# Optimization experiments

Hardware: AMD Instinct MI355X
Metric: run time of the kernel (lower is better)

## Reference

```python
import jax, jax.numpy as jnp
import numpy as np

LOWER_CURV = -0.22703196
UPPER_CURV = 0.36853024
N_NODES = 50000
N_EDGES = 400000
KSIZE = 5            # kernel_size per dim
KTOT = KSIZE ** 3    # 125 weight matrices (dim=3)
DIMS = [1, 8, 16, 16, 8, 1]
# corner bit patterns for degree-1 B-spline in 3D: [8,3]
_BITS = np.array([[(s >> d) & 1 for d in range(3)] for s in range(8)], dtype=np.int32)


def transform(x, rng=10.0):
    t = (x - LOWER_CURV) / (UPPER_CURV - LOWER_CURV) * (2.0 * rng) - rng
    return jnp.clip(t, -rng, rng)


def spline_basis(pseudo):
    # pseudo: [E,3] in [0,1]. Degree-1 open B-spline, kernel_size=5 per dim.
    pos = jnp.clip(pseudo, 0.0, 1.0) * (KSIZE - 1)                  # [E,3]
    k0 = jnp.clip(jnp.floor(pos), 0, KSIZE - 2).astype(jnp.int32)   # [E,3]
    frac = pos - k0.astype(pos.dtype)                               # [E,3]
    bits = jnp.asarray(_BITS)                                       # [8,3]
    # basis[e,s] = prod_d (frac_d if bit else 1-frac_d)
    basis = jnp.prod(jnp.where(bits[None, :, :] == 1, frac[:, None, :], 1.0 - frac[:, None, :]), axis=-1)  # [E,8]
    idx = k0[:, None, :] + bits[None, :, :]                         # [E,8,3]
    wi = idx[..., 0] * (KSIZE * KSIZE) + idx[..., 1] * KSIZE + idx[..., 2]  # [E,8] in [0,125)
    return basis, wi


def spline_conv(x, src, dst, basis, wi, weight, root, bias):
    # x: [N,Cin]; weight: [125,Cin,Cout]; sum aggregation (norm=False)
    n, cin = x.shape
    xs = x[src]                                          # [E,Cin] gather
    contrib = basis[..., None] * xs[:, None, :]          # [E,8,Cin]
    seg = (dst[:, None] * KTOT + wi).reshape(-1)         # [8E] combined (node,kernel) id
    h = jax.ops.segment_sum(contrib.reshape(-1, cin), seg, num_segments=n * KTOT)
    out = jnp.einsum('vki,kio->vo', h.reshape(n, KTOT, cin), weight)
    return out + x @ root + bias


def setup_inputs() -> dict:
    key = jax.random.key(0)
    ks = jax.random.split(key, 20)
    inp = {}
    inp['x'] = jax.random.normal(ks[0], (N_NODES, 1), dtype=jnp.float32) * 0.2
    inp['edge_index'] = jax.random.randint(ks[1], (2, N_EDGES), 0, N_NODES, dtype=jnp.int32)
    inp['edge_attr'] = jax.random.uniform(ks[2], (N_EDGES, 3), dtype=jnp.float32)
    for l in range(5):
        cin, cout = DIMS[l], DIMS[l + 1]
        inp[f'w{l+1}'] = jax.random.normal(ks[3 + 3 * l], (KTOT, cin, cout), dtype=jnp.float32) / np.sqrt(8.0 * cin)
        inp[f'root{l+1}'] = jax.random.normal(ks[4 + 3 * l], (cin, cout), dtype=jnp.float32) / np.sqrt(float(cin))
        inp[f'b{l+1}'] = jnp.zeros((cout,), dtype=jnp.float32)
    return inp


def reference(x, edge_index, edge_attr, w1, root1, b1, w2, root2, b2, w3, root3, b3, w4, root4, b4, w5, root5, b5):
    src, dst = edge_index[0], edge_index[1]
    basis, wi = spline_basis(edge_attr)
    h = transform(x, 10.0)
    for (w, r, b) in ((w1, root1, b1), (w2, root2, b2), (w3, root3, b3), (w4, root4, b4), (w5, root5, b5)):
        h = jax.nn.elu(spline_conv(h, src, dst, basis, wi, w, r, b))
    return h.reshape(-1)
```

## Files before the change

kernel.cpp:

```cpp
#include <hip/hip_runtime.h>
#include <math.h>

#define KSIZE 5
#define KTOT 125
#define CHUNK 2048

static constexpr float LOWER_CURV = -0.22703196f;
static constexpr float UPPER_CURV = 0.36853024f;

typedef _Float16 h2 __attribute__((ext_vector_type(2)));
typedef _Float16 h8_t __attribute__((ext_vector_type(8)));
typedef float f32x4 __attribute__((ext_vector_type(4)));

__device__ __forceinline__ unsigned pack_u32(float a, float b) {
    return __builtin_bit_cast(unsigned, __builtin_amdgcn_cvt_pkrtz(a, b));
}

__host__ __device__ static inline int cdiv(int a, int b) { return (a + b - 1) / b; }

__device__ __forceinline__ void unpack_bb10(unsigned w1, float bb[8]) {
    const float s = 1.0f / 1023.0f;
    float f0 = (float)(w1 & 1023u) * s;
    float f1 = (float)((w1 >> 10) & 1023u) * s;
    float f2 = (float)((w1 >> 20) & 1023u) * s;
    float a0 = 1.f - f0, a1 = 1.f - f1, a2 = 1.f - f2;
    float p00 = a0 * a1, p10 = f0 * a1, p01 = a0 * f1, p11 = f0 * f1;
    bb[0] = p00 * a2; bb[1] = p10 * a2; bb[2] = p01 * a2; bb[3] = p11 * a2;
    bb[4] = p00 * f2; bb[5] = p10 * f2; bb[6] = p01 * f2; bb[7] = p11 * f2;
}

__device__ __forceinline__ void spline_wf(const float* __restrict__ a3,
                                          int& wib, float fr[3]) {
    int k[3];
#pragma unroll
    for (int d = 0; d < 3; ++d) {
        float p = fminf(fmaxf(a3[d], 0.f), 1.f) * 4.f;
        float f0 = fminf(floorf(p), 3.f);
        k[d] = (int)f0;
        fr[d] = p - f0;
    }
    wib = k[0] * 25 + k[1] * 5 + k[2];
}


__global__ void zero_counts(int* __restrict__ p, int n) {
    int i = blockIdx.x * blockDim.x + threadIdx.x;
    if (i < n) p[i] = 0;
}

__global__ __launch_bounds__(256) void hist_tr(
        const float* __restrict__ x, float* __restrict__ h,
        const int* __restrict__ dst, const float* __restrict__ attr,
        int* __restrict__ counts, int* __restrict__ bcnt, int N, int E) {
    __shared__ int lh[KTOT];
    const int tid = threadIdx.x;
    for (int i = tid; i < KTOT; i += 256) lh[i] = 0;
    __syncthreads();
    int i = blockIdx.x * 256 + tid;
    if (i < N) {
        float t = (x[i] - LOWER_CURV) / (UPPER_CURV - LOWER_CURV) * 20.0f - 10.0f;
        h[i] = fminf(fmaxf(t, -10.0f), 10.0f);
    }
    const int base = blockIdx.x * CHUNK;
#pragma unroll
    for (int k = 0; k < 8; ++k) {
        int e = base + tid + k * 256;
        if (e < E) {
            atomicAdd(&counts[dst[e]], 1);
            float a3[3] = {attr[e * 3], attr[e * 3 + 1], attr[e * 3 + 2]};
            int wib; float fr[3];
            spline_wf(a3, wib, fr);
            atomicAdd(&lh[wib], 1);
        }
    }
    __syncthreads();
    for (int j = tid; j < KTOT; j += 256) {
        int c = lh[j];
        if (c) atomicAdd(&bcnt[j], c);
    }
}

__global__ void scan_blocks(const int* __restrict__ counts, int* __restrict__ rowptr,
                            int* __restrict__ bsums, int n) {
    __shared__ int sh[256];
    int tid = threadIdx.x;
    int i = blockIdx.x * 256 + tid;
    int v = (i < n) ? counts[i] : 0;
    sh[tid] = v;
    __syncthreads();
    for (int off = 1; off < 256; off <<= 1) {
        int t = (tid >= off) ? sh[tid - off] : 0;
        __syncthreads();
        sh[tid] += t;
        __syncthreads();
    }
    if (i < n) rowptr[i] = sh[tid] - v;
    if (tid == 255) bsums[blockIdx.x] = sh[255];
}

__global__ void add_offsets2(int* __restrict__ rowptr, const int* __restrict__ bsums,
                             int* __restrict__ cursor, const int* __restrict__ bcnt,
                             int* __restrict__ bases, int* __restrict__ bcursor,
                             int nb, int n, int E) {
    __shared__ int sh[256];
    __shared__ int sb[128];
    int tid = threadIdx.x;
    int v = (tid < nb) ? bsums[tid] : 0;
    sh[tid] = v;
    __syncthreads();
    for (int off = 1; off < 256; off <<= 1) {
        int t = (tid >= off) ? sh[tid - off] : 0;
        __syncthreads();
        sh[tid] += t;
        __syncthreads();
    }
    int boff = (blockIdx.x == 0) ? 0 : sh[blockIdx.x - 1];
    int i = blockIdx.x * 256 + tid;
    if (i < n) {
        int r = rowptr[i] + boff;
        rowptr[i] = r;
        cursor[i] = r;
    }
    if (i == 0) rowptr[n] = E;
    if (blockIdx.x == 0) {
        int cap = 0;
        if (tid < 128) {
            cap = (tid < KTOT) ? ((bcnt[tid] + 15) & ~15) : 0;
            sb[tid] = cap;
        }
        __syncthreads();
        for (int off = 1; off < 128; off <<= 1) {
            int t = (tid >= off && tid < 128) ? sb[tid - off] : 0;
            __syncthreads();
            if (tid < 128) sb[tid] += t;
            __syncthreads();
        }
        if (tid < KTOT) {
            int excl = sb[tid] - cap;
            bases[tid] = excl;
            bcursor[tid] = excl;
            if (tid == KTOT - 1) bases[KTOT] = excl + cap;
        }
    }
}

__global__ __launch_bounds__(256) void scatter_prep(
        const int* __restrict__ src, const int* __restrict__ dst,
        const float* __restrict__ attr, int* __restrict__ cursor,
        int* __restrict__ bcursor, const int* __restrict__ bcnt,
        const int* __restrict__ bases,
        uint2* __restrict__ records, uint2* __restrict__ records_d,
        int* __restrict__ iperm, int E, int nchunk, int nprep,
        const float* __restrict__ W2, const float* __restrict__ W3,
        const float* __restrict__ W4, _Float16* __restrict__ wh2,
        _Float16* __restrict__ wh3, _Float16* __restrict__ wh4) {
    __shared__ int lh[KTOT], lbase[KTOT], lrank[KTOT];
    const int tid = threadIdx.x;

    if ((int)blockIdx.x >= nchunk + nprep) {
        int b = (int)blockIdx.x - nchunk - nprep;
        int s = bases[b] + bcnt[b];
        int e = bases[b + 1];
        for (int i = s + tid; i < e; i += 256) {
            records[i] = make_uint2((unsigned)b << 18, 0u);
            iperm[i] = E;
        }
        return;
    }
    if ((int)blockIdx.x >= nchunk) {
        int idx = ((int)blockIdx.x - nchunk) * 256 + tid;
        if (idx >= 80000) return;
        if (idx < 16000) {
            int wi = idx / 128, q = idx % 128;
            int i = q / 16, o = q % 16;
            wh2[wi * 128 + o * 8 + i] = (_Float16)W2[idx];
        } else if (idx < 48000) {
            int r = idx - 16000;
            int wi = r / 256, q = r % 256;
            int i = q / 16, o = q % 16;
            wh3[wi * 256 + (i >> 3) * 128 + o * 8 + (i & 7)] = (_Float16)W3[r];
        } else {
            int r = idx - 48000;
            int wi = r / 256, q = r % 256;
            int i = q / 16, o = q % 16;
            float val = (o < 8) ? W4[(wi * 16 + i) * 8 + o] : 0.0f;
            wh4[wi * 256 + (i >> 3) * 128 + o * 8 + (i & 7)] = (_Float16)val;
        }
        return;
    }

    for (int i = tid; i < KTOT; i += 256) { lh[i] = 0; lrank[i] = 0; }
    __syncthreads();
    const int base = blockIdx.x * CHUNK;

    int wibs[8]; unsigned w1s[8];
#pragma unroll
    for (int k = 0; k < 8; ++k) {
        int e = base + tid + k * 256;
        wibs[k] = -1;
        if (e < E) {
            float a3[3] = {attr[e * 3], attr[e * 3 + 1], attr[e * 3 + 2]};
            int wib; float fr[3];
            spline_wf(a3, wib, fr);
            wibs[k] = wib;
            unsigned q0 = (unsigned)__float2int_rn(fr[0] * 1023.f);
            unsigned q1 = (unsigned)__float2int_rn(fr[1] * 1023.f);
            unsigned q2 = (unsigned)__float2int_rn(fr[2] * 1023.f);
            w1s[k] = q0 | (q1 << 10) | (q2 << 20);
            atomicAdd(&lh[wib], 1);
        }
    }
    __syncthreads();
    for (int i = tid; i < KTOT; i += 256) {
        int c = lh[i];
        lbase[i] = c ? atomicAdd(&bcursor[i], c) : 0;
    }
    __syncthreads();
#pragma unroll
    for (int k = 0; k < 8; ++k) {
        int e = base + tid + k * 256;
        if (e < E) {
            int w = wibs[k];
            int pos = lbase[w] + atomicAdd(&lrank[w], 1);
            uint2 rec = make_uint2((unsigned)src[e] | ((unsigned)w << 18), w1s[k]);
            records[pos] = rec;
            int p = atomicAdd(&cursor[dst[e]], 1);
            iperm[pos] = p;
            records_d[p] = rec;
        }
    }
}

template<int Cin, int CR>
__global__ __launch_bounds__(512) void edge_gemm_mfma(
        const uint2* __restrict__ records, const unsigned* __restrict__ xh,
        const _Float16* __restrict__ Wg, const int* __restrict__ iperm,
        _Float16* __restrict__ y, const int* __restrict__ epad_ptr) {
    constexpr int Cout = 16;
    constexpr int CC = Cin * Cout;
    constexpr int WH = KTOT * CC;
    constexpr int NM = Cin / 4;
    __shared__ __align__(16) _Float16 Wl[WH];
    for (int t = threadIdx.x; t < WH / 8; t += 512)
        ((uint4*)Wl)[t] = ((const uint4*)Wg)[t];
    __syncthreads();

    const int Ep = *epad_ptr;
    const int ntiles = Ep >> 4;
    const int lane = threadIdx.x & 63;
    const int o = lane & 15;
    const int kb = lane >> 4;
    const int chunk = (Cin == 16) ? (kb & 1) : 0;
    const int wid = blockIdx.x * 8 + (threadIdx.x >> 6);
    const int nwaves = gridDim.x * 8;
    constexpr int TAP[8] = {0, 25, 5, 30, 1, 26, 6, 31};

    for (int tile = wid; tile < ntiles; tile += nwaves) {
        const int tb = tile << 4;
        uint2 rec = records[tb + o];
        const int wib = (int)(((unsigned)__builtin_amdgcn_readfirstlane((int)rec.x)) >> 18);
        float bb[8];
        unpack_bb10(rec.y, bb);
        const unsigned sn = rec.x & 0x3FFFFu;
        uint4 xq = *(const uint4*)(xh + (size_t)sn * (Cin / 2) + chunk * 4);
        h2 xv[4];
        xv[0] = __builtin_bit_cast(h2, xq.x);
        xv[1] = __builtin_bit_cast(h2, xq.y);
        xv[2] = __builtin_bit_cast(h2, xq.z);
        xv[3] = __builtin_bit_cast(h2, xq.w);

        f32x4 acc = {0.f, 0.f, 0.f, 0.f};
#pragma unroll
        for (int m = 0; m < NM; ++m) {
            const int t = (Cin == 16) ? (2 * m + (kb >> 1)) : (4 * m + kb);
            const int wi = wib + TAP[t];
            _Float16 sh = (_Float16)bb[t];
            h2 ss; ss[0] = sh; ss[1] = sh;
            union { h8_t v; h2 h[4]; uint4 q; } A, B;
            A.h[0] = xv[0] * ss; A.h[1] = xv[1] * ss;
            A.h[2] = xv[2] * ss; A.h[3] = xv[3] * ss;
            B.q = *(const uint4*)&Wl[wi * CC + chunk * (8 * Cout) + o * 8];
            acc = __builtin_amdgcn_mfma_f32_16x16x32_f16(A.v, B.v, acc, 0, 0, 0);
        }
        if (CR == 16 || o < CR) {
#pragma unroll
            for (int r = 0; r < 4; ++r) {
                int dp = iperm[tb + kb * 4 + r];
                y[(size_t)dp * CR + o] = (_Float16)acc[r];
            }
        }
    }
}

template<int Cin, int Cout>
__global__ void node_reduce(const int* __restrict__ rowptr,
                            const unsigned* __restrict__ yu,
                            const float* __restrict__ x,
                            const float* __restrict__ root,
                            const float* __restrict__ bias,
                            float* __restrict__ out, unsigned* __restrict__ xh,
                            int N) {
    constexpr int C2 = Cout / 2;
    int t = blockIdx.x * blockDim.x + threadIdx.x;
    int v = t / C2, o2 = t % C2;
    if (v >= N) return;
    int beg = rowptr[v], end = rowptr[v + 1];
    float a0 = 0.f, a1 = 0.f;
    for (int p = beg; p < end; ++p) {
        h2 hh = __builtin_bit_cast(h2, yu[(size_t)p * C2 + o2]);
        a0 += (float)hh[0];
        a1 += (float)hh[1];
    }
    const int o = 2 * o2;
    a0 += bias[o]; a1 += bias[o + 1];
#pragma unroll
    for (int i = 0; i < Cin; ++i) {
        float xv = x[(size_t)v * Cin + i];
        a0 = fmaf(xv, root[i * Cout + o], a0);
        a1 = fmaf(xv, root[i * Cout + o + 1], a1);
    }
    a0 = a0 > 0.f ? a0 : expm1f(a0);
    a1 = a1 > 0.f ? a1 : expm1f(a1);
    ((float2*)out)[(size_t)v * C2 + o2] = make_float2(a0, a1);
    xh[(size_t)v * C2 + o2] = pack_u32(a0, a1);
}


__global__ __launch_bounds__(512) void agg_l1(
        const int* __restrict__ rowptr, const uint2* __restrict__ records_d,
        const float* __restrict__ x, const float* __restrict__ W,
        const float* __restrict__ root, const float* __restrict__ bias,
        float* __restrict__ out, unsigned* __restrict__ xh2,
        int N, int totalWaves) {
    const int lane = threadIdx.x & 63;
    const int o = lane & 7;
    const int slot = lane >> 3;
    const int wid = blockIdx.x * 8 + (threadIdx.x >> 6);
    constexpr int TAP[8] = {0, 25, 5, 30, 1, 26, 6, 31};

    for (int v = wid; v < N; v += totalWaves) {
        const int beg = rowptr[v], end = rowptr[v + 1];
        float acc = 0.0f;
        for (int p0 = beg; p0 < end; p0 += 8) {
            const int p = p0 + slot;
            float xv = 0.f, bb[8];
            int wib = 0;
#pragma unroll
            for (int t = 0; t < 8; ++t) bb[t] = 0.f;
            if (p < end) {
                uint2 rec = records_d[p];
                unpack_bb10(rec.y, bb);
                wib = (int)(rec.x >> 18);
                xv = x[rec.x & 0x3FFFFu];
            }
#pragma unroll
            for (int t = 0; t < 8; ++t)
                acc = fmaf(bb[t] * xv, __ldg(&W[(wib + TAP[t]) * 8 + o]), acc);
        }
#pragma unroll
        for (int m = 8; m < 64; m <<= 1) acc += __shfl_xor(acc, m);
        if (slot == 0) {
            float z = acc + bias[o] + x[v] * root[o];
            z = z > 0.0f ? z : expm1f(z);
            out[(size_t)v * 8 + o] = z;
            float zp = __shfl_xor(z, 1);
            if ((o & 1) == 0) xh2[(size_t)v * 4 + (o >> 1)] = pack_u32(z, zp);
        }
    }
}

__global__ __launch_bounds__(512) void agg_l5(
        const int* __restrict__ rowptr, const uint2* __restrict__ records_d,
        const float* __restrict__ x, const float* __restrict__ W,
        const float* __restrict__ root, const float* __restrict__ bias,
        float* __restrict__ out, int N, int totalWaves) {
    const int lane = threadIdx.x & 63;
    const int i = lane & 7;
    const int slot = lane >> 3;
    const int wid = blockIdx.x * 8 + (threadIdx.x >> 6);
    constexpr int TAP[8] = {0, 25, 5, 30, 1, 26, 6, 31};

    for (int v = wid; v < N; v += totalWaves) {
        const int beg = rowptr[v], end = rowptr[v + 1];
        float acc = 0.0f;
        for (int p0 = beg; p0 < end; p0 += 8) {
            const int p = p0 + slot;
            float xi = 0.f, bb[8];
            int wib = 0;
#pragma unroll
            for (int t = 0; t < 8; ++t) bb[t] = 0.f;
            if (p < end) {
                uint2 rec = records_d[p];
                unpack_bb10(rec.y, bb);
                wib = (int)(rec.x >> 18);
                xi = x[(size_t)(rec.x & 0x3FFFFu) * 8 + i];
            }
#pragma unroll
            for (int t = 0; t < 8; ++t)
                acc = fmaf(bb[t] * xi, __ldg(&W[(wib + TAP[t]) * 8 + i]), acc);
        }
        if (slot == 0) acc = fmaf(x[(size_t)v * 8 + i], root[i], acc);
#pragma unroll
        for (int m = 1; m < 64; m <<= 1) acc += __shfl_xor(acc, m);
        if (lane == 0) {
            float z = acc + bias[0];
            out[v] = z > 0.0f ? z : expm1f(z);
        }
    }
}


static inline char* align256(char* p) {
    return (char*)(((uintptr_t)p + 255) & ~(uintptr_t)255);
}

extern "C" void kernel_launch(void* const* d_in, const int* in_sizes, int n_in,
                              void* d_out, int out_size, void* d_ws, size_t ws_size,
                              hipStream_t stream) {
    const float* x    = (const float*)d_in[0];
    const int*   ei   = (const int*)d_in[1];
    const float* attr = (const float*)d_in[2];
    const float* w[5]    = {(const float*)d_in[3],  (const float*)d_in[6],
                            (const float*)d_in[9],  (const float*)d_in[12],
                            (const float*)d_in[15]};
    const float* root[5] = {(const float*)d_in[4],  (const float*)d_in[7],
                            (const float*)d_in[10], (const float*)d_in[13],
                            (const float*)d_in[16]};
    const float* bias[5] = {(const float*)d_in[5],  (const float*)d_in[8],
                            (const float*)d_in[11], (const float*)d_in[14],
                            (const float*)d_in[17]};

    const int N = in_sizes[0];
    const int E = in_sizes[1] / 2;
    const int* src = ei;
    const int* dst = ei + E;
    const int EPCAP = E + 2048;

    char* ws = (char*)d_ws;
    float* bufA      = (float*)ws;    ws = align256(ws + (size_t)N * 16 * 4);
    float* bufB      = (float*)ws;    ws = align256(ws + (size_t)N * 16 * 4);
    int*   counts    = (int*)ws;      ws = align256(ws + (size_t)(N + 128) * 4);
    int*   bcnt      = counts + N;
    int*   cursor    = (int*)ws;      ws = align256(ws + (size_t)N * 4);
    int*   rowptr    = (int*)ws;      ws = align256(ws + (size_t)(N + 1) * 4);
    int*   bsums     = (int*)ws;      ws = align256(ws + 256 * 4);
    int*   bases     = (int*)ws;      ws = align256(ws + 128 * 4);
    int*   bcursor   = (int*)ws;      ws = align256(ws + 128 * 4);
    uint2* records   = (uint2*)ws;    ws = align256(ws + (size_t)EPCAP * 8);
    uint2* records_d = (uint2*)ws;    ws = align256(ws + (size_t)E * 8);
    int*   iperm     = (int*)ws;      ws = align256(ws + (size_t)EPCAP * 4);
    _Float16* y      = (_Float16*)ws; ws = align256(ws + (size_t)(E + 16) * 16 * 2);
    unsigned* xhA    = (unsigned*)ws; ws = align256(ws + (size_t)N * 8 * 4);
    unsigned* xhB    = (unsigned*)ws; ws = align256(ws + (size_t)N * 8 * 4);
    _Float16* wh2    = (_Float16*)ws; ws = align256(ws + (size_t)KTOT * 8 * 16 * 2);
    _Float16* wh3    = (_Float16*)ws; ws = align256(ws + (size_t)KTOT * 16 * 16 * 2);
    _Float16* wh4    = (_Float16*)ws; ws = align256(ws + (size_t)KTOT * 16 * 16 * 2);

    const int B = 256;
    const int nb = cdiv(N, 256);
    const int nchunk = cdiv(E, CHUNK);
    const int nprep = cdiv(80000, 256);
    const int* epad = bases + KTOT;
    const unsigned* yu = (const unsigned*)y;

    zero_counts<<<cdiv(N + 128, B), B, 0, stream>>>(counts, N + 128);
    hist_tr<<<nchunk, 256, 0, stream>>>(x, bufA, dst, attr, counts, bcnt, N, E);
    scan_blocks<<<nb, 256, 0, stream>>>(counts, rowptr, bsums, N);
    add_offsets2<<<nb, 256, 0, stream>>>(rowptr, bsums, cursor, bcnt, bases,
                                         bcursor, nb, N, E);
    scatter_prep<<<nchunk + nprep + KTOT, 256, 0, stream>>>(
        src, dst, attr, cursor, bcursor, bcnt, bases,
        records, records_d, iperm, E, nchunk, nprep,
        w[1], w[2], w[3], wh2, wh3, wh4);

    const int GB = 512, TW = GB * 8;

    agg_l1<<<GB, 512, 0, stream>>>(rowptr, records_d, bufA, w[0],
                                   root[0], bias[0], bufB, xhA, N, TW);
    edge_gemm_mfma<8, 16><<<GB, 512, 0, stream>>>(records, xhA, wh2, iperm, y, epad);
    node_reduce<8, 16><<<cdiv(N * 8, B), B, 0, stream>>>(rowptr, yu, bufB,
                                                         root[1], bias[1], bufA, xhB, N);
    edge_gemm_mfma<16, 16><<<GB, 512, 0, stream>>>(records, xhB, wh3, iperm, y, epad);
    node_reduce<16, 16><<<cdiv(N * 8, B), B, 0, stream>>>(rowptr, yu, bufA,
                                                          root[2], bias[2], bufB, xhA, N);
    edge_gemm_mfma<16, 8><<<GB, 512, 0, stream>>>(records, xhA, wh4, iperm, y, epad);
    node_reduce<16, 8><<<cdiv(N * 4, B), B, 0, stream>>>(rowptr, yu, bufB,
                                                         root[3], bias[3], bufA, xhB, N);
    agg_l5<<<GB, 512, 0, stream>>>(rowptr, records_d, bufA, w[4],
                                   root[4], bias[4], (float*)d_out, N, TW);
}
```

Baseline: 175.5 us.

## Replace dst-sorted agg kernels for layers 1 and 5 with edge-then-reduce passes

Drops the dst-ordered records_d copy and its scattered write in scatter_prep. Layers 1 and 5 now use the same scheme as the middle layers: an edge-parallel kernel over the kernel-bucketed records writes per-edge messages through iperm, then a node reduce over rowptr sums them. This removes the per-node wave loops, which were badly load-balanced and read W through scattered global loads, and keeps the weights in LDS instead. The cost is an extra kernel launch per layer plus a round trip of intermediate messages through global memory, with fp16 rounding of the layer-1 messages and fp16 inputs and weights in layer 5.

```diff
diff --git a/kernel.cpp b/kernel.cpp
--- a/kernel.cpp
+++ b/kernel.cpp
@@ -14,6 +14,13 @@
 
 __device__ __forceinline__ unsigned pack_u32(float a, float b) {
     return __builtin_bit_cast(unsigned, __builtin_amdgcn_cvt_pkrtz(a, b));
+}
+__device__ __forceinline__ float fdot2f(h2 a, h2 b, float c) {
+#if __has_builtin(__builtin_amdgcn_fdot2)
+    return __builtin_amdgcn_fdot2(a, b, c, false);
+#else
+    return c + (float)a[0] * (float)b[0] + (float)a[1] * (float)b[1];
+#endif
 }
 
 __host__ __device__ static inline int cdiv(int a, int b) { return (a + b - 1) / b; }
@@ -149,8 +156,8 @@
         const float* __restrict__ attr, int* __restrict__ cursor,
         int* __restrict__ bcursor, const int* __restrict__ bcnt,
         const int* __restrict__ bases,
-        uint2* __restrict__ records, uint2* __restrict__ records_d,
-        int* __restrict__ iperm, int E, int nchunk, int nprep,
+        uint2* __restrict__ records, int* __restrict__ iperm,
+        int E, int nchunk, int nprep,
         const float* __restrict__ W2, const float* __restrict__ W3,
         const float* __restrict__ W4, _Float16* __restrict__ wh2,
         _Float16* __restrict__ wh3, _Float16* __restrict__ wh4) {
@@ -222,13 +229,99 @@
         if (e < E) {
             int w = wibs[k];
             int pos = lbase[w] + atomicAdd(&lrank[w], 1);
-            uint2 rec = make_uint2((unsigned)src[e] | ((unsigned)w << 18), w1s[k]);
-            records[pos] = rec;
-            int p = atomicAdd(&cursor[dst[e]], 1);
-            iperm[pos] = p;
-            records_d[p] = rec;
-        }
-    }
+            records[pos] = make_uint2((unsigned)src[e] | ((unsigned)w << 18), w1s[k]);
+            iperm[pos] = atomicAdd(&cursor[dst[e]], 1);
+        }
+    }
+}
+
+__global__ __launch_bounds__(512) void l1_edge(
+        const uint2* __restrict__ records, const float* __restrict__ h,
+        const float* __restrict__ W1,
+        const int* __restrict__ iperm, _Float16* __restrict__ y,
+        const int* __restrict__ epad_ptr) {
+    __shared__ float Wl[KTOT * 8];
+    for (int i = threadIdx.x; i < KTOT * 8; i += 512) Wl[i] = W1[i];
+    __syncthreads();
+    const int Ep = *epad_ptr;
+    const int stride = gridDim.x * 512;
+    constexpr int TAP[8] = {0, 25, 5, 30, 1, 26, 6, 31};
+    for (int idx = blockIdx.x * 512 + threadIdx.x; idx < Ep; idx += stride) {
+        uint2 rec = records[idx];
+        float bb[8];
+        unpack_bb10(rec.y, bb);
+        const int wib = (int)(rec.x >> 18);
+        float xv = h[rec.x & 0x3FFFFu];
+        float s[8];
+#pragma unroll
+        for (int o = 0; o < 8; ++o) s[o] = 0.f;
+#pragma unroll
+        for (int t = 0; t < 8; ++t) {
+            const float* wp = &Wl[(wib + TAP[t]) * 8];
+#pragma unroll
+            for (int o = 0; o < 8; ++o) s[o] = fmaf(bb[t], wp[o], s[o]);
+        }
+        uint4 pk;
+        pk.x = pack_u32(xv * s[0], xv * s[1]);
+        pk.y = pack_u32(xv * s[2], xv * s[3]);
+        pk.z = pack_u32(xv * s[4], xv * s[5]);
+        pk.w = pack_u32(xv * s[6], xv * s[7]);
+        int dp = iperm[idx];
+        *(uint4*)&y[(size_t)dp * 8] = pk;
+    }
+}
+
+__global__ __launch_bounds__(512) void l5_edge(
+        const uint2* __restrict__ records, const unsigned* __restrict__ xh,
+        const float* __restrict__ W5,
+        const int* __restrict__ iperm, float* __restrict__ y5,
+        const int* __restrict__ epad_ptr) {
+    __shared__ h2 Wl[KTOT * 4];
+    for (int i = threadIdx.x; i < KTOT * 4; i += 512)
+        Wl[i] = __builtin_bit_cast(h2, pack_u32(W5[2 * i], W5[2 * i + 1]));
+    __syncthreads();
+    const int Ep = *epad_ptr;
+    const int stride = gridDim.x * 512;
+    constexpr int TAP[8] = {0, 25, 5, 30, 1, 26, 6, 31};
+    for (int idx = blockIdx.x * 512 + threadIdx.x; idx < Ep; idx += stride) {
+        uint2 rec = records[idx];
+        float bb[8];
+        unpack_bb10(rec.y, bb);
+        const int wib = (int)(rec.x >> 18);
+        uint4 xq = *(const uint4*)(xh + (size_t)(rec.x & 0x3FFFFu) * 4);
+        h2 hx[4];
+        hx[0] = __builtin_bit_cast(h2, xq.x);
+        hx[1] = __builtin_bit_cast(h2, xq.y);
+        hx[2] = __builtin_bit_cast(h2, xq.z);
+        hx[3] = __builtin_bit_cast(h2, xq.w);
+        float acc = 0.f;
+#pragma unroll
+        for (int t = 0; t < 8; ++t) {
+            const h2* wp = &Wl[(wib + TAP[t]) * 4];
+            float dot = 0.f;
+            dot = fdot2f(hx[0], wp[0], dot);
+            dot = fdot2f(hx[1], wp[1], dot);
+            dot = fdot2f(hx[2], wp[2], dot);
+            dot = fdot2f(hx[3], wp[3], dot);
+            acc = fmaf(bb[t], dot, acc);
+        }
+        y5[iperm[idx]] = acc;
+    }
+}
+
+__global__ void node_fin5(const int* __restrict__ rowptr, const float* __restrict__ y5,
+                          const float* __restrict__ x,
+                          const float* __restrict__ root, const float* __restrict__ bias,
+                          float* __restrict__ out, int N) {
+    int v = blockIdx.x * blockDim.x + threadIdx.x;
+    if (v >= N) return;
+    int beg = rowptr[v], end = rowptr[v + 1];
+    float acc = bias[0];
+    for (int p = beg; p < end; ++p) acc += y5[p];
+#pragma unroll
+    for (int i = 0; i < 8; ++i)
+        acc = fmaf(x[(size_t)v * 8 + i], root[i], acc);
+    out[v] = acc > 0.f ? acc : expm1f(acc);
 }
 
 template<int Cin, int CR>
@@ -326,90 +419,6 @@
 }
 
 
-__global__ __launch_bounds__(512) void agg_l1(
-        const int* __restrict__ rowptr, const uint2* __restrict__ records_d,
-        const float* __restrict__ x, const float* __restrict__ W,
-        const float* __restrict__ root, const float* __restrict__ bias,
-        float* __restrict__ out, unsigned* __restrict__ xh2,
-        int N, int totalWaves) {
-    const int lane = threadIdx.x & 63;
-    const int o = lane & 7;
-    const int slot = lane >> 3;
-    const int wid = blockIdx.x * 8 + (threadIdx.x >> 6);
-    constexpr int TAP[8] = {0, 25, 5, 30, 1, 26, 6, 31};
-
-    for (int v = wid; v < N; v += totalWaves) {
-        const int beg = rowptr[v], end = rowptr[v + 1];
-        float acc = 0.0f;
-        for (int p0 = beg; p0 < end; p0 += 8) {
-            const int p = p0 + slot;
-            float xv = 0.f, bb[8];
-            int wib = 0;
-#pragma unroll
-            for (int t = 0; t < 8; ++t) bb[t] = 0.f;
-            if (p < end) {
-                uint2 rec = records_d[p];
-                unpack_bb10(rec.y, bb);
-                wib = (int)(rec.x >> 18);
-                xv = x[rec.x & 0x3FFFFu];
-            }
-#pragma unroll
-            for (int t = 0; t < 8; ++t)
-                acc = fmaf(bb[t] * xv, __ldg(&W[(wib + TAP[t]) * 8 + o]), acc);
-        }
-#pragma unroll
-        for (int m = 8; m < 64; m <<= 1) acc += __shfl_xor(acc, m);
-        if (slot == 0) {
-            float z = acc + bias[o] + x[v] * root[o];
-            z = z > 0.0f ? z : expm1f(z);
-            out[(size_t)v * 8 + o] = z;
-            float zp = __shfl_xor(z, 1);
-            if ((o & 1) == 0) xh2[(size_t)v * 4 + (o >> 1)] = pack_u32(z, zp);
-        }
-    }
-}
-
-__global__ __launch_bounds__(512) void agg_l5(
-        const int* __restrict__ rowptr, const uint2* __restrict__ records_d,
-        const float* __restrict__ x, const float* __restrict__ W,
-        const float* __restrict__ root, const float* __restrict__ bias,
-        float* __restrict__ out, int N, int totalWaves) {
-    const int lane = threadIdx.x & 63;
-    const int i = lane & 7;
-    const int slot = lane >> 3;
-    const int wid = blockIdx.x * 8 + (threadIdx.x >> 6);
-    constexpr int TAP[8] = {0, 25, 5, 30, 1, 26, 6, 31};
-
-    for (int v = wid; v < N; v += totalWaves) {
-        const int beg = rowptr[v], end = rowptr[v + 1];
-        float acc = 0.0f;
-        for (int p0 = beg; p0 < end; p0 += 8) {
-            const int p = p0 + slot;
-            float xi = 0.f, bb[8];
-            int wib = 0;
-#pragma unroll
-            for (int t = 0; t < 8; ++t) bb[t] = 0.f;
-            if (p < end) {
-                uint2 rec = records_d[p];
-                unpack_bb10(rec.y, bb);
-                wib = (int)(rec.x >> 18);
-                xi = x[(size_t)(rec.x & 0x3FFFFu) * 8 + i];
-            }
-#pragma unroll
-            for (int t = 0; t < 8; ++t)
-                acc = fmaf(bb[t] * xi, __ldg(&W[(wib + TAP[t]) * 8 + i]), acc);
-        }
-        if (slot == 0) acc = fmaf(x[(size_t)v * 8 + i], root[i], acc);
-#pragma unroll
-        for (int m = 1; m < 64; m <<= 1) acc += __shfl_xor(acc, m);
-        if (lane == 0) {
-            float z = acc + bias[0];
-            out[v] = z > 0.0f ? z : expm1f(z);
-        }
-    }
-}
-
-
 static inline char* align256(char* p) {
     return (char*)(((uintptr_t)p + 255) & ~(uintptr_t)255);
 }
@@ -447,7 +456,6 @@
     int*   bases     = (int*)ws;      ws = align256(ws + 128 * 4);
     int*   bcursor   = (int*)ws;      ws = align256(ws + 128 * 4);
     uint2* records   = (uint2*)ws;    ws = align256(ws + (size_t)EPCAP * 8);
-    uint2* records_d = (uint2*)ws;    ws = align256(ws + (size_t)E * 8);
     int*   iperm     = (int*)ws;      ws = align256(ws + (size_t)EPCAP * 4);
     _Float16* y      = (_Float16*)ws; ws = align256(ws + (size_t)(E + 16) * 16 * 2);
     unsigned* xhA    = (unsigned*)ws; ws = align256(ws + (size_t)N * 8 * 4);
@@ -462,6 +470,7 @@
     const int nprep = cdiv(80000, 256);
     const int* epad = bases + KTOT;
     const unsigned* yu = (const unsigned*)y;
+    float* y5 = (float*)y;
 
     zero_counts<<<cdiv(N + 128, B), B, 0, stream>>>(counts, N + 128);
     hist_tr<<<nchunk, 256, 0, stream>>>(x, bufA, dst, attr, counts, bcnt, N, E);
@@ -470,13 +479,14 @@
                                          bcursor, nb, N, E);
     scatter_prep<<<nchunk + nprep + KTOT, 256, 0, stream>>>(
         src, dst, attr, cursor, bcursor, bcnt, bases,
-        records, records_d, iperm, E, nchunk, nprep,
+        records, iperm, E, nchunk, nprep,
         w[1], w[2], w[3], wh2, wh3, wh4);
 
-    const int GB = 512, TW = GB * 8;
-
-    agg_l1<<<GB, 512, 0, stream>>>(rowptr, records_d, bufA, w[0],
-                                   root[0], bias[0], bufB, xhA, N, TW);
+    const int GB = 512;
+
+    l1_edge<<<GB, 512, 0, stream>>>(records, bufA, w[0], iperm, y, epad);
+    node_reduce<1, 8><<<cdiv(N * 4, B), B, 0, stream>>>(rowptr, yu, bufA,
+                                                        root[0], bias[0], bufB, xhA, N);
     edge_gemm_mfma<8, 16><<<GB, 512, 0, stream>>>(records, xhA, wh2, iperm, y, epad);
     node_reduce<8, 16><<<cdiv(N * 8, B), B, 0, stream>>>(rowptr, yu, bufB,
                                                          root[1], bias[1], bufA, xhB, N);
@@ -486,6 +496,7 @@
     edge_gemm_mfma<16, 8><<<GB, 512, 0, stream>>>(records, xhA, wh4, iperm, y, epad);
     node_reduce<16, 8><<<cdiv(N * 4, B), B, 0, stream>>>(rowptr, yu, bufB,
                                                          root[3], bias[3], bufA, xhB, N);
-    agg_l5<<<GB, 512, 0, stream>>>(rowptr, records_d, bufA, w[4],
-                                   root[4], bias[4], (float*)d_out, N, TW);
-}
+    l5_edge<<<GB, 512, 0, stream>>>(records, xhB, w[4], iperm, y5, epad);
+    node_fin5<<<cdiv(N, B), B, 0, stream>>>(rowptr, y5, bufA, root[4], bias[4],
+                                            (float*)d_out, N);
+}
```

Measured after the change: 154.7 us. -11.8%, faster.
